# Kernel tuning notes

Measured on AMD Instinct MI355X. Metric: run time of the kernel, lower is better.

The kernel has to match this reference:

```python
import jax, jax.numpy as jnp
import numpy as np

D_MODEL, NUM_HEADS, ROPE_DIM = 256, 8, 16
B_GRAPHS, N_MAX = 16, 512


def _make_batch():
    # ragged graph sizes between 256 and 512 atoms; contiguous, sorted ids
    sizes = np.array([256 + (i * 256) // 15 for i in range(B_GRAPHS)], dtype=np.int64)
    return np.repeat(np.arange(B_GRAPHS), sizes)  # total N = 6137


def setup_inputs() -> dict:
    key = jax.random.key(0)
    ks = jax.random.split(key, 6)
    batch_np = _make_batch()
    N = int(batch_np.shape[0])
    x = jax.random.normal(ks[0], (N, D_MODEL), jnp.float32)
    pos = jax.random.normal(ks[1], (N, 3), jnp.float32) * 3.0
    W_qkv = jax.random.normal(ks[2], (D_MODEL, 3 * D_MODEL), jnp.float32) / np.sqrt(D_MODEL).astype(np.float32)
    W_out = jax.random.normal(ks[3], (D_MODEL, D_MODEL), jnp.float32) / np.sqrt(D_MODEL).astype(np.float32)
    rope_freqs = jax.random.normal(ks[4], (ROPE_DIM,), jnp.float32) * 0.1
    W_rope = jax.random.normal(ks[5], (ROPE_DIM, NUM_HEADS), jnp.float32) / np.sqrt(ROPE_DIM).astype(np.float32)
    gamma = jnp.ones((D_MODEL,), jnp.float32)
    beta = jnp.zeros((D_MODEL,), jnp.float32)
    return {"x": x, "pos": pos, "batch": jnp.asarray(batch_np, jnp.int32),
            "W_qkv": W_qkv, "W_out": W_out, "rope_freqs": rope_freqs,
            "W_rope": W_rope, "gamma": gamma, "beta": beta,
            "B": B_GRAPHS, "n_max": N_MAX}


def _forward(x, pos, W_qkv, W_out, rope_freqs, W_rope, gamma, beta, batch, B, n_max):
    N, d = x.shape
    H = W_rope.shape[1]
    hd = d // H
    scale = hd ** -0.5
    # pad ragged graphs to [B, n_max] via vectorized scatter (batch is sorted)
    sizes = jax.ops.segment_sum(jnp.ones((N,), jnp.int32), batch, num_segments=B)
    offsets = jnp.concatenate([jnp.zeros((1,), jnp.int32), jnp.cumsum(sizes)[:-1].astype(jnp.int32)])
    pidx = jnp.arange(N, dtype=jnp.int32) - offsets[batch]  # position within graph
    x_pad = jnp.zeros((B, n_max, d), x.dtype).at[batch, pidx].set(x)
    pos_pad = jnp.zeros((B, n_max, 3), pos.dtype).at[batch, pidx].set(pos)
    pad = jnp.ones((B, n_max), bool).at[batch, pidx].set(False)  # True = padding
    # multi-head self-attention on scalar channel
    qkv = x_pad @ W_qkv  # [B, n, 3d]
    q, k, v = jnp.split(qkv, 3, axis=-1)
    heads = lambda t: t.reshape(B, n_max, H, hd).transpose(0, 2, 1, 3)  # [B,H,n,hd]
    q, k, v = heads(q), heads(k), heads(v)
    logits = jnp.einsum('bhid,bhjd->bhij', q, k) * scale
    # Euclidean RoPE distance bias: rope_proj(cos(|omega| * ||r_i - r_j||))
    diff = pos_pad[:, :, None, :] - pos_pad[:, None, :, :]  # [B,n,n,3]
    sq = jnp.sum(diff * diff, axis=-1)
    dist = jnp.where(sq > 0, jnp.sqrt(jnp.where(sq > 0, sq, 1.0)), 0.0)  # safe norm
    fourier = jnp.cos(dist[..., None] * jnp.abs(rope_freqs))  # [B,n,n,r]
    bias = jnp.einsum('bijr,rh->bhij', fourier, W_rope)
    pair_pad = (pad[:, :, None] | pad[:, None, :])[:, None]  # [B,1,n,n]
    bias = jnp.where(pair_pad, 0.0, bias)
    logits = jnp.where(pad[:, None, None, :], -1e9, logits + bias)
    attn = jax.nn.softmax(logits, axis=-1)
    out = jnp.einsum('bhij,bhjd->bhid', attn, v)
    out = out.transpose(0, 2, 1, 3).reshape(B, n_max, d) @ W_out
    out_flat = out[batch, pidx]  # gather back to flat node list
    # residual + LayerNorm (eps = 1e-5)
    y = x + out_flat
    mu = jnp.mean(y, axis=-1, keepdims=True)
    var = jnp.mean((y - mu) ** 2, axis=-1, keepdims=True)
    return gamma * (y - mu) * jax.lax.rsqrt(var + 1e-5) + beta


def reference(x, pos, batch, W_qkv, W_out, rope_freqs, W_rope, gamma, beta, B, n_max):
    return _forward(x, pos, W_qkv, W_out, rope_freqs, W_rope, gamma, beta, batch, B, n_max)
```

## Files before the change

kernel.cpp:

```cpp
#include <hip/hip_runtime.h>
#include <hip/hip_bf16.h>

typedef __hip_bfloat16 bf16;
typedef short bf16x8 __attribute__((ext_vector_type(8)));
typedef float f32x4 __attribute__((ext_vector_type(4)));

#define NGRAPH 16
#define QSCALE 0.17677669529663687f
#define VT_LD 8192

__global__ __launch_bounds__(256) void k_prep(const float* __restrict__ x,
                                              const float* __restrict__ Wqkv,
                                              const float* __restrict__ Wout,
                                              const int* __restrict__ batch,
                                              bf16* __restrict__ xb,
                                              bf16* __restrict__ Wqkv_t,
                                              bf16* __restrict__ Wout_t,
                                              int* __restrict__ offs, int N) {
  int tid = blockIdx.x * 256 + threadIdx.x;
  int T = gridDim.x * 256;
  for (int i = tid; i < N * 256; i += T) xb[i] = __float2bfloat16(x[i]);
  for (int i = tid; i < 768 * 256; i += T) {
    int n = i >> 8, k = i & 255;
    Wqkv_t[i] = __float2bfloat16(Wqkv[k * 768 + n]);
  }
  for (int i = tid; i < 256 * 256; i += T) {
    int n = i >> 8, k = i & 255;
    Wout_t[i] = __float2bfloat16(Wout[k * 256 + n]);
  }
  for (int i = tid; i < N; i += T) {
    if (i == 0) { offs[0] = 0; offs[NGRAPH] = N; }
    else if (batch[i] != batch[i - 1]) offs[batch[i]] = i;
  }
}

__global__ __launch_bounds__(256) void k_gemm_qkv(const bf16* __restrict__ A,
                                                  const bf16* __restrict__ Bt,
                                                  const int* __restrict__ batch,
                                                  const int* __restrict__ offs,
                                                  bf16* __restrict__ C,
                                                  bf16* __restrict__ VT, int M) {
  __shared__ float tr[64][65];
  __shared__ int rowcol[64];
  int t = threadIdx.x, w = t >> 6, l = t & 63, fr = l & 15, fq = l >> 4;
  int m0 = blockIdx.x * 64, n0 = blockIdx.y * 64;
  bool isV = (n0 >= 512);
  if (isV && t < 64) {
    int m = m0 + t; if (m > M - 1) m = M - 1;
    int b = batch[m];
    rowcol[t] = b * 512 + (m - offs[b]);
  }
  int arow = m0 + w * 16 + fr; if (arow > M - 1) arow = M - 1;
  bf16x8 af[8];
  #pragma unroll
  for (int kt = 0; kt < 8; ++kt)
    af[kt] = *(const bf16x8*)(A + (size_t)arow * 256 + kt * 32 + fq * 8);
  f32x4 acc[4];
  #pragma unroll
  for (int nt = 0; nt < 4; ++nt) acc[nt] = (f32x4){0.f, 0.f, 0.f, 0.f};
  #pragma unroll
  for (int nt = 0; nt < 4; ++nt) {
    int brow = n0 + nt * 16 + fr;
    #pragma unroll
    for (int kt = 0; kt < 8; ++kt) {
      bf16x8 bf_ = *(const bf16x8*)(Bt + (size_t)brow * 256 + kt * 32 + fq * 8);
      acc[nt] = __builtin_amdgcn_mfma_f32_16x16x32_bf16(af[kt], bf_, acc[nt], 0, 0, 0);
    }
  }
  #pragma unroll
  for (int nt = 0; nt < 4; ++nt) {
    int col = n0 + nt * 16 + fr;
    float sc = (col < 256) ? QSCALE : 1.f;
    #pragma unroll
    for (int rr = 0; rr < 4; ++rr) {
      int m = m0 + w * 16 + fq * 4 + rr;
      if (m < M) C[(size_t)m * 768 + col] = __float2bfloat16(acc[nt][rr] * sc);
    }
  }
  if (isV) {
    #pragma unroll
    for (int nt = 0; nt < 4; ++nt)
      #pragma unroll
      for (int rr = 0; rr < 4; ++rr)
        tr[nt * 16 + fr][w * 16 + fq * 4 + rr] = acc[nt][rr];
    __syncthreads();
    int c = t >> 2, r0 = (t & 3) * 16;
    int dg = (n0 - 512) + c;
    #pragma unroll
    for (int i = 0; i < 16; ++i) {
      int r = r0 + i;
      VT[(size_t)dg * VT_LD + rowcol[r]] = __float2bfloat16(tr[c][r]);
    }
  }
}

__global__ __launch_bounds__(256) void k_attn(const float* __restrict__ pos,
                                              const float* __restrict__ freqs,
                                              const float* __restrict__ Wrope,
                                              const bf16* __restrict__ QKVb,
                                              const bf16* __restrict__ VT,
                                              const int* __restrict__ offs,
                                              bf16* __restrict__ Ob) {
  __shared__ float Sb[2][4][16][34];
  __shared__ __align__(16) bf16 Pt[4][16][40];
  __shared__ float wf[16];
  __shared__ float Wr[16][4];
  int b = blockIdx.y, hbase = blockIdx.z * 4;
  int off = offs[b], n = offs[b + 1] - off;
  int q0 = blockIdx.x * 16;
  if (q0 >= n) return;
  int t = threadIdx.x, w = t >> 6, l = t & 63, fr = l & 15, fq = l >> 4;
  int h = hbase + w;
  if (t < 16) wf[t] = fabsf(freqs[t]);
  if (t < 64) Wr[t >> 2][t & 3] = Wrope[(t >> 2) * 8 + hbase + (t & 3)];
  int qrow = q0 + fr; bool qv = qrow < n;
  bf16x8 aq = *(const bf16x8*)(QKVb + (size_t)((qv ? off + qrow : off)) * 768 + h * 32 + fq * 8);
  if (!qv) aq = (bf16x8){0, 0, 0, 0, 0, 0, 0, 0};
  int bq = t >> 5, bj = t & 31;
  float qpx[2], qpy[2], qpz[2]; bool bqv[2];
  #pragma unroll
  for (int e = 0; e < 2; ++e) {
    int qq = q0 + bq + 8 * e; bqv[e] = qq < n;
    int a = (bqv[e] ? off + qq : off) * 3;
    qpx[e] = pos[a]; qpy[e] = pos[a + 1]; qpz[e] = pos[a + 2];
  }
  float m_st[4], l_st[4]; f32x4 Oa[2];
  #pragma unroll
  for (int rr = 0; rr < 4; ++rr) { m_st[rr] = -1e30f; l_st[rr] = 0.f; }
  Oa[0] = (f32x4){0.f, 0.f, 0.f, 0.f}; Oa[1] = (f32x4){0.f, 0.f, 0.f, 0.f};
  __syncthreads();

  int par = 0;
  for (int j0 = 0; j0 < n; j0 += 32, par ^= 1) {
    {
      int jg = j0 + bj; bool vj = jg < n;
      int a = (vj ? off + jg : off) * 3;
      float jx = pos[a], jy = pos[a + 1], jz = pos[a + 2];
      #pragma unroll
      for (int e = 0; e < 2; ++e) {
        float bv0 = 0.f, bv1 = 0.f, bv2 = 0.f, bv3 = 0.f;
        if (vj && bqv[e]) {
          float dx = qpx[e] - jx, dy = qpy[e] - jy, dz = qpz[e] - jz;
          float dist = sqrtf(dx * dx + dy * dy + dz * dz);
          #pragma unroll
          for (int r = 0; r < 16; ++r) {
            float cv = __cosf(dist * wf[r]);
            bv0 += cv * Wr[r][0]; bv1 += cv * Wr[r][1];
            bv2 += cv * Wr[r][2]; bv3 += cv * Wr[r][3];
          }
        }
        int qi = bq + 8 * e;
        Sb[par][0][qi][bj] = vj ? bv0 : -1e30f;
        Sb[par][1][qi][bj] = vj ? bv1 : -1e30f;
        Sb[par][2][qi][bj] = vj ? bv2 : -1e30f;
        Sb[par][3][qi][bj] = vj ? bv3 : -1e30f;
      }
    }
    __syncthreads();
    f32x4 Sv[2];
    #pragma unroll
    for (int jt = 0; jt < 2; ++jt) {
      int krow = j0 + jt * 16 + fr;
      bf16x8 bk = *(const bf16x8*)(QKVb + (size_t)((krow < n) ? off + krow : off) * 768 + 256 + h * 32 + fq * 8);
      f32x4 z = {0.f, 0.f, 0.f, 0.f};
      Sv[jt] = __builtin_amdgcn_mfma_f32_16x16x32_bf16(aq, bk, z, 0, 0, 0);
      #pragma unroll
      for (int rr = 0; rr < 4; ++rr) Sv[jt][rr] += Sb[par][w][fq * 4 + rr][jt * 16 + fr];
    }
    #pragma unroll
    for (int rr = 0; rr < 4; ++rr) {
      float mrow = fmaxf(Sv[0][rr], Sv[1][rr]);
      #pragma unroll
      for (int m2 = 1; m2 <= 8; m2 <<= 1) mrow = fmaxf(mrow, __shfl_xor(mrow, m2));
      float mnew = fmaxf(m_st[rr], mrow);
      float al = __expf(m_st[rr] - mnew);
      m_st[rr] = mnew;
      float p0 = __expf(Sv[0][rr] - mnew), p1 = __expf(Sv[1][rr] - mnew);
      Sv[0][rr] = p0; Sv[1][rr] = p1;
      float rs = p0 + p1;
      #pragma unroll
      for (int m2 = 1; m2 <= 8; m2 <<= 1) rs += __shfl_xor(rs, m2);
      l_st[rr] = l_st[rr] * al + rs;
      Oa[0][rr] *= al; Oa[1][rr] *= al;
    }
    #pragma unroll
    for (int jt = 0; jt < 2; ++jt)
      #pragma unroll
      for (int rr = 0; rr < 4; ++rr)
        Pt[w][fq * 4 + rr][jt * 16 + fr] = __float2bfloat16(Sv[jt][rr]);
    bf16x8 ap = *(const bf16x8*)&Pt[w][fr][fq * 8];
    #pragma unroll
    for (int dh = 0; dh < 2; ++dh) {
      bf16x8 bv = *(const bf16x8*)(VT + (size_t)(h * 32 + dh * 16 + fr) * VT_LD + b * 512 + j0 + fq * 8);
      Oa[dh] = __builtin_amdgcn_mfma_f32_16x16x32_bf16(ap, bv, Oa[dh], 0, 0, 0);
    }
  }
  #pragma unroll
  for (int dh = 0; dh < 2; ++dh)
    #pragma unroll
    for (int rr = 0; rr < 4; ++rr) {
      int row = q0 + fq * 4 + rr;
      if (row < n)
        Ob[(size_t)(off + row) * 256 + h * 32 + dh * 16 + fr] =
            __float2bfloat16(Oa[dh][rr] / l_st[rr]);
    }
}

__global__ __launch_bounds__(256) void k_gemm_out(const bf16* __restrict__ A,
                                                  const bf16* __restrict__ Bt,
                                                  float* __restrict__ C, int M) {
  int t = threadIdx.x, w = t >> 6, l = t & 63, fr = l & 15, fq = l >> 4;
  int m0 = blockIdx.x * 64, n0 = blockIdx.y * 64;
  int arow = m0 + w * 16 + fr; if (arow > M - 1) arow = M - 1;
  bf16x8 af[8];
  #pragma unroll
  for (int kt = 0; kt < 8; ++kt)
    af[kt] = *(const bf16x8*)(A + (size_t)arow * 256 + kt * 32 + fq * 8);
  f32x4 acc[4];
  #pragma unroll
  for (int nt = 0; nt < 4; ++nt) acc[nt] = (f32x4){0.f, 0.f, 0.f, 0.f};
  #pragma unroll
  for (int nt = 0; nt < 4; ++nt) {
    int brow = n0 + nt * 16 + fr;
    #pragma unroll
    for (int kt = 0; kt < 8; ++kt) {
      bf16x8 bf_ = *(const bf16x8*)(Bt + (size_t)brow * 256 + kt * 32 + fq * 8);
      acc[nt] = __builtin_amdgcn_mfma_f32_16x16x32_bf16(af[kt], bf_, acc[nt], 0, 0, 0);
    }
  }
  #pragma unroll
  for (int nt = 0; nt < 4; ++nt) {
    int col = n0 + nt * 16 + fr;
    #pragma unroll
    for (int rr = 0; rr < 4; ++rr) {
      int m = m0 + w * 16 + fq * 4 + rr;
      if (m < M) C[(size_t)m * 256 + col] = acc[nt][rr];
    }
  }
}

__global__ __launch_bounds__(256) void k_ln(const float* __restrict__ x,
                                            const float* __restrict__ Y,
                                            const float* __restrict__ gamma,
                                            const float* __restrict__ beta,
                                            float* __restrict__ out, int N) {
  int t = threadIdx.x;
  int w = t >> 6, lane = t & 63;
  int row = blockIdx.x * 4 + w;
  if (row >= N) return;
  float v[4];
  float s = 0.f, ss = 0.f;
  #pragma unroll
  for (int i = 0; i < 4; ++i) {
    int c = lane + 64 * i;
    v[i] = x[(size_t)row * 256 + c] + Y[(size_t)row * 256 + c];
    s += v[i]; ss += v[i] * v[i];
  }
  #pragma unroll
  for (int m = 32; m >= 1; m >>= 1) { s += __shfl_xor(s, m); ss += __shfl_xor(ss, m); }
  float mean = s * (1.f / 256.f);
  float var = ss * (1.f / 256.f) - mean * mean;
  float rstd = rsqrtf(var + 1e-5f);
  #pragma unroll
  for (int i = 0; i < 4; ++i) {
    int c = lane + 64 * i;
    out[(size_t)row * 256 + c] = gamma[c] * (v[i] - mean) * rstd + beta[c];
  }
}

extern "C" void kernel_launch(void* const* d_in, const int* in_sizes, int n_in,
                              void* d_out, int out_size, void* d_ws, size_t ws_size,
                              hipStream_t stream) {
  (void)n_in; (void)out_size; (void)ws_size;
  const float* x     = (const float*)d_in[0];
  const float* pos   = (const float*)d_in[1];
  const int*   batch = (const int*)d_in[2];
  const float* Wqkv  = (const float*)d_in[3];
  const float* Wout  = (const float*)d_in[4];
  const float* freqs = (const float*)d_in[5];
  const float* Wrope = (const float*)d_in[6];
  const float* gamma = (const float*)d_in[7];
  const float* beta  = (const float*)d_in[8];
  float* out = (float*)d_out;

  int N = in_sizes[0] / 256;

  char* base = (char*)d_ws;
  int*   offs   = (int*)base;
  bf16*  QKVb   = (bf16*)(base + 1024);
  bf16*  VT     = (bf16*)(base + 9427456);
  bf16*  xb     = (bf16*)(base + 13621760);
  bf16*  Wqkv_t = (bf16*)(base + 16763904);
  bf16*  Wout_t = (bf16*)(base + 17157120);
  float* Y      = (float*)(base + 17288192);
  bf16*  Ob     = xb;

  int MB = (N + 63) / 64;
  k_prep<<<1024, 256, 0, stream>>>(x, Wqkv, Wout, batch, xb, Wqkv_t, Wout_t, offs, N);
  k_gemm_qkv<<<dim3(MB, 12), 256, 0, stream>>>(xb, Wqkv_t, batch, offs, QKVb, VT, N);
  k_attn<<<dim3(32, NGRAPH, 2), 256, 0, stream>>>(pos, freqs, Wrope, QKVb, VT, offs, Ob);
  k_gemm_out<<<dim3(MB, 4), 256, 0, stream>>>(Ob, Wout_t, Y, N);
  k_ln<<<(N + 3) / 4, 256, 0, stream>>>(x, Y, gamma, beta, out, N);
}
```

Measured before the change: 190.4 us.

## Precompute RoPE distance bias in a separate kernel and fuse output GEMM with LayerNorm

Adds a k_bias kernel that computes the cos-Fourier distance bias for all 8 heads once per query/key tile and stores it as bf16 tiles in workspace. Previously each head group recomputed it inside attention. The attention kernel now reads the precomputed bias, prefetches the next key/value/bias tile into registers, and drops the online running-max softmax in favour of plain exp with a final normalisation. The output projection and the residual+LayerNorm are fused into one kernel that computes full 256-wide rows. The fast path costs a large bf16 bias buffer in memory traffic, is gated on workspace size, and the missing max subtraction risks overflow if logits grow large.

```diff
diff --git a/kernel.cpp b/kernel.cpp
--- a/kernel.cpp
+++ b/kernel.cpp
@@ -8,6 +8,8 @@
 #define NGRAPH 16
 #define QSCALE 0.17677669529663687f
 #define VT_LD 8192
+
+struct __align__(16) bf8x { bf16 v[8]; };
 
 __global__ __launch_bounds__(256) void k_prep(const float* __restrict__ x,
                                               const float* __restrict__ Wqkv,
@@ -31,6 +33,66 @@
   for (int i = tid; i < N; i += T) {
     if (i == 0) { offs[0] = 0; offs[NGRAPH] = N; }
     else if (batch[i] != batch[i - 1]) offs[batch[i]] = i;
+  }
+}
+
+__global__ __launch_bounds__(256) void k_bias(const float* __restrict__ pos,
+                                              const float* __restrict__ freqs,
+                                              const float* __restrict__ Wrope,
+                                              const int* __restrict__ offs,
+                                              bf16* __restrict__ bias) {
+  __shared__ float Sb[8][16][33];
+  __shared__ float wf[16];
+  __shared__ float Wr[16][8];
+  int b = blockIdx.z;
+  int off = offs[b], n = offs[b + 1] - off;
+  int q0 = blockIdx.x * 16, j0 = blockIdx.y * 32;
+  if (q0 >= n || j0 >= n) return;
+  int t = threadIdx.x;
+  if (t < 16) wf[t] = fabsf(freqs[t]);
+  if (t < 128) Wr[t >> 3][t & 7] = Wrope[t];
+  int tb = 0;
+  for (int g = 0; g < b; ++g) {
+    int ng = offs[g + 1] - offs[g];
+    tb += ((ng + 15) >> 4) * ((ng + 31) >> 5);
+  }
+  int jtiles = (n + 31) >> 5;
+  bf16* tile = bias + (size_t)(tb + (q0 >> 4) * jtiles + (j0 >> 5)) * 4096;
+  int qs = t >> 5, j = t & 31;
+  int jg = j0 + j; bool vj = jg < n;
+  float jx, jy, jz;
+  { int a = (vj ? off + jg : off) * 3; jx = pos[a]; jy = pos[a + 1]; jz = pos[a + 2]; }
+  __syncthreads();
+  #pragma unroll
+  for (int e = 0; e < 2; ++e) {
+    int q = qs + 8 * e; int qg = q0 + q; bool vq = qg < n;
+    float bv[8];
+    #pragma unroll
+    for (int h = 0; h < 8; ++h) bv[h] = 0.f;
+    if (vq && vj) {
+      int a = (off + qg) * 3;
+      float dx = pos[a] - jx, dy = pos[a + 1] - jy, dz = pos[a + 2] - jz;
+      float dist = sqrtf(dx * dx + dy * dy + dz * dz);
+      #pragma unroll
+      for (int r = 0; r < 16; ++r) {
+        float cv = __cosf(dist * wf[r]);
+        #pragma unroll
+        for (int h = 0; h < 8; ++h) bv[h] += cv * Wr[r][h];
+      }
+    }
+    #pragma unroll
+    for (int h = 0; h < 8; ++h) Sb[h][q][j] = (vq && vj) ? bv[h] : -1e30f;
+  }
+  __syncthreads();
+  int w = t >> 6, l = t & 63, fq = l >> 4, fr = l & 15;
+  #pragma unroll
+  for (int hh = 0; hh < 2; ++hh) {
+    int h = w * 2 + hh;
+    __align__(16) bf16 pk[8];
+    #pragma unroll
+    for (int k = 0; k < 8; ++k)
+      pk[k] = __float2bfloat16(Sb[h][fq * 4 + (k & 3)][(k >> 2) * 16 + fr]);
+    *(bf16x8*)(tile + h * 512 + l * 8) = *(const bf16x8*)pk;
   }
 }
 
@@ -94,13 +156,88 @@
   }
 }
 
-__global__ __launch_bounds__(256) void k_attn(const float* __restrict__ pos,
-                                              const float* __restrict__ freqs,
-                                              const float* __restrict__ Wrope,
-                                              const bf16* __restrict__ QKVb,
+__global__ __launch_bounds__(256) void k_attn(const bf16* __restrict__ QKVb,
                                               const bf16* __restrict__ VT,
+                                              const bf16* __restrict__ bias,
                                               const int* __restrict__ offs,
                                               bf16* __restrict__ Ob) {
+  __shared__ __align__(16) bf16 Pt[4][16][40];
+  int b = blockIdx.y, hbase = blockIdx.z * 4;
+  int off = offs[b], n = offs[b + 1] - off;
+  int q0 = blockIdx.x * 16;
+  if (q0 >= n) return;
+  int t = threadIdx.x, w = t >> 6, l = t & 63, fr = l & 15, fq = l >> 4;
+  int h = hbase + w;
+  int tb = 0;
+  for (int g = 0; g < b; ++g) {
+    int ng = offs[g + 1] - offs[g];
+    tb += ((ng + 15) >> 4) * ((ng + 31) >> 5);
+  }
+  int jtiles = (n + 31) >> 5;
+  const bf16* btile = bias + (size_t)(tb + (q0 >> 4) * jtiles) * 4096 + h * 512 + l * 8;
+  const bf16* Kb = QKVb + (size_t)off * 768 + 256 + h * 32 + fq * 8;
+  const bf16* Vb = VT + (size_t)(h * 32 + fr) * VT_LD + b * 512 + fq * 8;
+  int qrow = q0 + fr; bool qv = qrow < n;
+  bf16x8 aq = *(const bf16x8*)(QKVb + (size_t)(qv ? off + qrow : off) * 768 + h * 32 + fq * 8);
+  if (!qv) aq = (bf16x8){0, 0, 0, 0, 0, 0, 0, 0};
+  f32x4 Oa[2];
+  Oa[0] = (f32x4){0.f, 0.f, 0.f, 0.f}; Oa[1] = (f32x4){0.f, 0.f, 0.f, 0.f};
+  float lacc[4] = {0.f, 0.f, 0.f, 0.f};
+
+#define LOADT(JT, B_, K0_, K1_, V0_, V1_) do {                                   \
+    int _jt = (JT); int _k0 = _jt * 32 + fr, _k1 = _k0 + 16;                     \
+    B_ = *(const bf8x*)(btile + (size_t)_jt * 4096);                             \
+    K0_ = *(const bf16x8*)(Kb + (size_t)((_k0 < n) ? _k0 : 0) * 768);            \
+    K1_ = *(const bf16x8*)(Kb + (size_t)((_k1 < n) ? _k1 : 0) * 768);            \
+    V0_ = *(const bf16x8*)(Vb + _jt * 32);                                       \
+    V1_ = *(const bf16x8*)(Vb + (size_t)16 * VT_LD + _jt * 32);                  \
+  } while (0)
+
+  bf8x cb; bf16x8 ck0, ck1, cv0, cv1;
+  LOADT(0, cb, ck0, ck1, cv0, cv1);
+  for (int jt = 0; jt < jtiles; ++jt) {
+    bf8x nb; bf16x8 nk0, nk1, nv0, nv1;
+    if (jt + 1 < jtiles) LOADT(jt + 1, nb, nk0, nk1, nv0, nv1);
+    f32x4 z = {0.f, 0.f, 0.f, 0.f};
+    f32x4 S0 = __builtin_amdgcn_mfma_f32_16x16x32_bf16(aq, ck0, z, 0, 0, 0);
+    f32x4 S1 = __builtin_amdgcn_mfma_f32_16x16x32_bf16(aq, ck1, z, 0, 0, 0);
+    #pragma unroll
+    for (int k = 0; k < 8; ++k) {
+      int jti = k >> 2, rr = k & 3;
+      float s = (jti ? S1[rr] : S0[rr]) + __bfloat162float(cb.v[k]);
+      float p = __expf(s);
+      lacc[rr] += p;
+      Pt[w][fq * 4 + rr][jti * 16 + fr] = __float2bfloat16(p);
+    }
+    bf16x8 ap = *(const bf16x8*)&Pt[w][fr][fq * 8];
+    Oa[0] = __builtin_amdgcn_mfma_f32_16x16x32_bf16(ap, cv0, Oa[0], 0, 0, 0);
+    Oa[1] = __builtin_amdgcn_mfma_f32_16x16x32_bf16(ap, cv1, Oa[1], 0, 0, 0);
+    cb = nb; ck0 = nk0; ck1 = nk1; cv0 = nv0; cv1 = nv1;
+  }
+#undef LOADT
+  #pragma unroll
+  for (int rr = 0; rr < 4; ++rr) {
+    #pragma unroll
+    for (int m2 = 1; m2 <= 8; m2 <<= 1) lacc[rr] += __shfl_xor(lacc[rr], m2);
+  }
+  #pragma unroll
+  for (int dh = 0; dh < 2; ++dh)
+    #pragma unroll
+    for (int rr = 0; rr < 4; ++rr) {
+      int row = q0 + fq * 4 + rr;
+      if (row < n)
+        Ob[(size_t)(off + row) * 256 + h * 32 + dh * 16 + fr] =
+            __float2bfloat16(Oa[dh][rr] / lacc[rr]);
+    }
+}
+
+__global__ __launch_bounds__(256) void k_attn_fb(const float* __restrict__ pos,
+                                                 const float* __restrict__ freqs,
+                                                 const float* __restrict__ Wrope,
+                                                 const bf16* __restrict__ QKVb,
+                                                 const bf16* __restrict__ VT,
+                                                 const int* __restrict__ offs,
+                                                 bf16* __restrict__ Ob) {
   __shared__ float Sb[2][4][16][34];
   __shared__ __align__(16) bf16 Pt[4][16][40];
   __shared__ float wf[16];
@@ -129,7 +266,6 @@
   for (int rr = 0; rr < 4; ++rr) { m_st[rr] = -1e30f; l_st[rr] = 0.f; }
   Oa[0] = (f32x4){0.f, 0.f, 0.f, 0.f}; Oa[1] = (f32x4){0.f, 0.f, 0.f, 0.f};
   __syncthreads();
-
   int par = 0;
   for (int j0 = 0; j0 < n; j0 += 32, par ^= 1) {
     {
@@ -206,72 +342,61 @@
     }
 }
 
-__global__ __launch_bounds__(256) void k_gemm_out(const bf16* __restrict__ A,
-                                                  const bf16* __restrict__ Bt,
-                                                  float* __restrict__ C, int M) {
+__global__ __launch_bounds__(256) void k_gemm_out_ln(const bf16* __restrict__ A,
+                                                     const bf16* __restrict__ Bt,
+                                                     const float* __restrict__ x,
+                                                     const float* __restrict__ gamma,
+                                                     const float* __restrict__ beta,
+                                                     float* __restrict__ out, int M) {
   int t = threadIdx.x, w = t >> 6, l = t & 63, fr = l & 15, fq = l >> 4;
-  int m0 = blockIdx.x * 64, n0 = blockIdx.y * 64;
+  int m0 = blockIdx.x * 64;
   int arow = m0 + w * 16 + fr; if (arow > M - 1) arow = M - 1;
   bf16x8 af[8];
   #pragma unroll
   for (int kt = 0; kt < 8; ++kt)
     af[kt] = *(const bf16x8*)(A + (size_t)arow * 256 + kt * 32 + fq * 8);
-  f32x4 acc[4];
-  #pragma unroll
-  for (int nt = 0; nt < 4; ++nt) acc[nt] = (f32x4){0.f, 0.f, 0.f, 0.f};
-  #pragma unroll
-  for (int nt = 0; nt < 4; ++nt) {
-    int brow = n0 + nt * 16 + fr;
+  f32x4 acc[16];
+  #pragma unroll
+  for (int nt = 0; nt < 16; ++nt) {
+    acc[nt] = (f32x4){0.f, 0.f, 0.f, 0.f};
+    int brow = nt * 16 + fr;
     #pragma unroll
     for (int kt = 0; kt < 8; ++kt) {
       bf16x8 bf_ = *(const bf16x8*)(Bt + (size_t)brow * 256 + kt * 32 + fq * 8);
       acc[nt] = __builtin_amdgcn_mfma_f32_16x16x32_bf16(af[kt], bf_, acc[nt], 0, 0, 0);
     }
   }
-  #pragma unroll
-  for (int nt = 0; nt < 4; ++nt) {
-    int col = n0 + nt * 16 + fr;
-    #pragma unroll
-    for (int rr = 0; rr < 4; ++rr) {
-      int m = m0 + w * 16 + fq * 4 + rr;
-      if (m < M) C[(size_t)m * 256 + col] = acc[nt][rr];
-    }
-  }
-}
-
-__global__ __launch_bounds__(256) void k_ln(const float* __restrict__ x,
-                                            const float* __restrict__ Y,
-                                            const float* __restrict__ gamma,
-                                            const float* __restrict__ beta,
-                                            float* __restrict__ out, int N) {
-  int t = threadIdx.x;
-  int w = t >> 6, lane = t & 63;
-  int row = blockIdx.x * 4 + w;
-  if (row >= N) return;
-  float v[4];
-  float s = 0.f, ss = 0.f;
-  #pragma unroll
-  for (int i = 0; i < 4; ++i) {
-    int c = lane + 64 * i;
-    v[i] = x[(size_t)row * 256 + c] + Y[(size_t)row * 256 + c];
-    s += v[i]; ss += v[i] * v[i];
-  }
-  #pragma unroll
-  for (int m = 32; m >= 1; m >>= 1) { s += __shfl_xor(s, m); ss += __shfl_xor(ss, m); }
-  float mean = s * (1.f / 256.f);
-  float var = ss * (1.f / 256.f) - mean * mean;
-  float rstd = rsqrtf(var + 1e-5f);
-  #pragma unroll
-  for (int i = 0; i < 4; ++i) {
-    int c = lane + 64 * i;
-    out[(size_t)row * 256 + c] = gamma[c] * (v[i] - mean) * rstd + beta[c];
+  float g[16], bb[16];
+  #pragma unroll
+  for (int nt = 0; nt < 16; ++nt) { g[nt] = gamma[nt * 16 + fr]; bb[nt] = beta[nt * 16 + fr]; }
+  #pragma unroll
+  for (int rr = 0; rr < 4; ++rr) {
+    int row = m0 + w * 16 + fq * 4 + rr;
+    int rc = (row < M) ? row : (M - 1);
+    float vv[16];
+    float s = 0.f, ss = 0.f;
+    #pragma unroll
+    for (int nt = 0; nt < 16; ++nt) {
+      float y = acc[nt][rr] + x[(size_t)rc * 256 + nt * 16 + fr];
+      vv[nt] = y; s += y; ss += y * y;
+    }
+    #pragma unroll
+    for (int m2 = 1; m2 <= 8; m2 <<= 1) { s += __shfl_xor(s, m2); ss += __shfl_xor(ss, m2); }
+    float mean = s * (1.f / 256.f);
+    float var = ss * (1.f / 256.f) - mean * mean;
+    float rstd = rsqrtf(var + 1e-5f);
+    if (row < M) {
+      #pragma unroll
+      for (int nt = 0; nt < 16; ++nt)
+        out[(size_t)row * 256 + nt * 16 + fr] = g[nt] * (vv[nt] - mean) * rstd + bb[nt];
+    }
   }
 }
 
 extern "C" void kernel_launch(void* const* d_in, const int* in_sizes, int n_in,
                               void* d_out, int out_size, void* d_ws, size_t ws_size,
                               hipStream_t stream) {
-  (void)n_in; (void)out_size; (void)ws_size;
+  (void)n_in; (void)out_size;
   const float* x     = (const float*)d_in[0];
   const float* pos   = (const float*)d_in[1];
   const int*   batch = (const int*)d_in[2];
@@ -292,13 +417,19 @@
   bf16*  xb     = (bf16*)(base + 13621760);
   bf16*  Wqkv_t = (bf16*)(base + 16763904);
   bf16*  Wout_t = (bf16*)(base + 17157120);
-  float* Y      = (float*)(base + 17288192);
+  bf16*  biasb  = (bf16*)(base + 17288192);
   bf16*  Ob     = xb;
+
+  bool fast = ws_size >= (size_t)58700000;
 
   int MB = (N + 63) / 64;
   k_prep<<<1024, 256, 0, stream>>>(x, Wqkv, Wout, batch, xb, Wqkv_t, Wout_t, offs, N);
+  if (fast)
+    k_bias<<<dim3(32, 16, NGRAPH), 256, 0, stream>>>(pos, freqs, Wrope, offs, biasb);
   k_gemm_qkv<<<dim3(MB, 12), 256, 0, stream>>>(xb, Wqkv_t, batch, offs, QKVb, VT, N);
-  k_attn<<<dim3(32, NGRAPH, 2), 256, 0, stream>>>(pos, freqs, Wrope, QKVb, VT, offs, Ob);
-  k_gemm_out<<<dim3(MB, 4), 256, 0, stream>>>(Ob, Wout_t, Y, N);
-  k_ln<<<(N + 3) / 4, 256, 0, stream>>>(x, Y, gamma, beta, out, N);
-}
+  if (fast)
+    k_attn<<<dim3(32, NGRAPH, 2), 256, 0, stream>>>(QKVb, VT, biasb, offs, Ob);
+  else
+    k_attn_fb<<<dim3(32, NGRAPH, 2), 256, 0, stream>>>(pos, freqs, Wrope, QKVb, VT, offs, Ob);
+  k_gemm_out_ln<<<MB, 256, 0, stream>>>(Ob, Wout_t, x, gamma, beta, out, N);
+}
```

New measurement: 205.4 us. 7.9% more time.
